# Performance work log

Measured on AMD Instinct MI355X. Metric: run time of the kernel, lower is better.

## Reference

```python
import jax, jax.numpy as jnp
import numpy as np

H = 16  # num_heads

def setup_inputs() -> dict:
    key = jax.random.key(0)
    ks = jax.random.split(key, 6)
    B, T, C, S = 2, 2048, 1024, 2048
    return {
        "q": jax.random.normal(ks[0], (B, T, C), jnp.float32),
        "k_xl": jax.random.normal(ks[1], (B, S, C), jnp.float32),
        "v_xl": jax.random.normal(ks[2], (B, S, C), jnp.float32),
        "W_qkv": jax.random.normal(ks[3], (3 * C, C), jnp.float32) * (1.0 / np.sqrt(C)),
        "W_proj": jax.random.normal(ks[4], (C, C), jnp.float32) * (1.0 / np.sqrt(C)),
        "pos_emb": jax.random.normal(ks[5], (S, C), jnp.float32),
        "is_causal": 0,
    }

def reference(q, k_xl, v_xl, W_qkv, W_proj, pos_emb, is_causal):
    B, T, C = q.shape
    hd = C // H
    # self_attention: W_qkv(q).split(d_model, -1)
    qkv = jnp.einsum('btc,dc->btd', q, W_qkv)  # [B,T,3C]
    qn, kn, vn = jnp.split(qkv, 3, axis=-1)
    # XL cache gets positional embedding added before use
    kx = k_xl + pos_emb[None, :, :]            # [B,S,C]
    vx = v_xl

    def to_heads(x):
        b, s, c = x.shape
        return x.reshape(b, s, H, hd).transpose(0, 2, 1, 3)  # [B,H,s,hd]

    qh = to_heads(qn)
    kcat = jnp.concatenate([to_heads(kx), to_heads(kn)], axis=2)  # [B,H,S+T,hd]
    vcat = jnp.concatenate([to_heads(vx), to_heads(vn)], axis=2)
    scale = 1.0 / jnp.sqrt(jnp.asarray(hd, qh.dtype))
    scores = jnp.einsum('bhtd,bhsd->bhts', qh, kcat) * scale  # [B,H,T,S+T]
    attn = jax.nn.softmax(scores, axis=-1)
    y = jnp.einsum('bhts,bhsd->bhtd', attn, vcat)  # [B,H,T,hd]
    y = y.transpose(0, 2, 1, 3).reshape(B, T, C)
    return jnp.einsum('btc,dc->btd', y, W_proj)
```

## Files before the change

### kernel.cpp

```cpp
#include <hip/hip_runtime.h>

typedef unsigned short u16;
typedef unsigned int u32;
typedef u16 u16x4 __attribute__((ext_vector_type(4)));
typedef u16 u16x8 __attribute__((ext_vector_type(8)));
typedef __bf16 bf16x8 __attribute__((ext_vector_type(8)));
typedef float f32x4 __attribute__((ext_vector_type(4)));
typedef float f32x16 __attribute__((ext_vector_type(16)));

static __device__ __forceinline__ u16 f2bf(float f) {
  union { float f; u32 u; } x; x.f = f;
  u32 r = x.u + 0x7fffu + ((x.u >> 16) & 1u);
  return (u16)(r >> 16);
}
static __device__ __forceinline__ u32 packbf(float a, float b) {
  union { u32 u; __bf16 h[2]; } x; x.h[0] = (__bf16)a; x.h[1] = (__bf16)b; return x.u;
}
static __device__ __forceinline__ void pl32swap(u32& a, u32& b) {
  asm volatile("v_permlane32_swap_b32 %0, %1" : "+v"(a), "+v"(b));
}
static __device__ __forceinline__ void gload16(const void* g, void* l) {
  __builtin_amdgcn_global_load_lds((const __attribute__((address_space(1))) unsigned int*)g,
                                   (__attribute__((address_space(3))) unsigned int*)l, 16, 0, 0);
}

__global__ __launch_bounds__(256) void cvt_fuse(const float* __restrict__ q, const float* __restrict__ wqkv_f,
                                                const float* __restrict__ wproj_f, const float* __restrict__ k_xl,
                                                const float* __restrict__ pos, u16* __restrict__ qbf,
                                                u16* __restrict__ wqkv, u16* __restrict__ wproj,
                                                u16* __restrict__ khxl, float sc) {
  int i = blockIdx.x * 256 + threadIdx.x;
  if (i < 2097152) {
    const float* src;
    u16* dst;
    int j;
    float s = 1.0f;
    if (i < 1048576) { src = q; dst = qbf; j = i; }
    else if (i < 1835008) { j = i - 1048576; src = wqkv_f; dst = wqkv; if (j < 262144) s = sc; }
    else { j = i - 1835008; src = wproj_f; dst = wproj; }
    float4 v = reinterpret_cast<const float4*>(src)[j];
    u16x4 o; o[0] = f2bf(v.x * s); o[1] = f2bf(v.y * s); o[2] = f2bf(v.z * s); o[3] = f2bf(v.w * s);
    reinterpret_cast<u16x4*>(dst)[j] = o;
  } else {
    int idx = i - 2097152;
    int d8 = idx & 7;
    int s = (idx >> 3) & 2047;
    int bh = idx >> 14;
    int b = bh >> 4, h = bh & 15;
    size_t src = ((size_t)(b * 2048 + s)) * 1024 + h * 64 + d8 * 8;
    size_t ps = ((size_t)s) * 1024 + h * 64 + d8 * 8;
    float4 a0 = *(const float4*)&k_xl[src];
    float4 a1 = *(const float4*)&k_xl[src + 4];
    float4 p0 = *(const float4*)&pos[ps];
    float4 p1 = *(const float4*)&pos[ps + 4];
    u16x8 o;
    o[0] = f2bf(a0.x + p0.x); o[1] = f2bf(a0.y + p0.y); o[2] = f2bf(a0.z + p0.z); o[3] = f2bf(a0.w + p0.w);
    o[4] = f2bf(a1.x + p1.x); o[5] = f2bf(a1.y + p1.y); o[6] = f2bf(a1.z + p1.z); o[7] = f2bf(a1.w + p1.w);
    *(u16x8*)&khxl[((size_t)bh * 2048 + s) * 64 + d8 * 8] = o;
  }
}

template <int OUT_BF16>
__global__ __launch_bounds__(256, 2) void gemm_bt3(const u16* __restrict__ A, const u16* __restrict__ B,
                                                   void* __restrict__ Cout, int M, int N, int K) {
  __shared__ alignas(128) u16 As[2][8192];
  __shared__ alignas(128) u16 Bs[2][8192];
  const int tid = threadIdx.x;
  const int m0 = blockIdx.y * 128, n0 = blockIdx.x * 128;
  const int wid = tid >> 6, lane = tid & 63;
  const int lm = lane & 15, lg = lane >> 4;
  const int wm = (wid >> 1) * 64, wn = (wid & 1) * 64;
  int srow[4], scol[4], dsto[4];
#pragma unroll
  for (int i = 0; i < 4; i++) {
    int li = tid + i * 256;
    srow[i] = li >> 3;
    scol[i] = ((li & 7) ^ (srow[i] & 7)) * 8;
    dsto[i] = (i * 256 + wid * 64) * 8;
  }
  f32x4 acc[4][4] = {};
#pragma unroll
  for (int i = 0; i < 4; i++) {
    gload16(&A[(size_t)(m0 + srow[i]) * K + scol[i]], &As[0][dsto[i]]);
    gload16(&B[(size_t)(n0 + srow[i]) * K + scol[i]], &Bs[0][dsto[i]]);
  }
  int cur = 0;
  for (int k0 = 0; k0 < K; k0 += 64) {
    __syncthreads();
    if (k0 + 64 < K) {
#pragma unroll
      for (int i = 0; i < 4; i++) {
        gload16(&A[(size_t)(m0 + srow[i]) * K + k0 + 64 + scol[i]], &As[cur ^ 1][dsto[i]]);
        gload16(&B[(size_t)(n0 + srow[i]) * K + k0 + 64 + scol[i]], &Bs[cur ^ 1][dsto[i]]);
      }
    }
    const u16* Asb = As[cur];
    const u16* Bsb = Bs[cur];
#pragma unroll
    for (int ks = 0; ks < 2; ks++) {
      bf16x8 af[4], bfr[4];
#pragma unroll
      for (int mi = 0; mi < 4; mi++) {
        int row = wm + mi * 16 + lm;
        af[mi] = *(const bf16x8*)&Asb[row * 64 + (((ks * 4 + lg) ^ (row & 7)) << 3)];
      }
#pragma unroll
      for (int ni = 0; ni < 4; ni++) {
        int row = wn + ni * 16 + lm;
        bfr[ni] = *(const bf16x8*)&Bsb[row * 64 + (((ks * 4 + lg) ^ (row & 7)) << 3)];
      }
#pragma unroll
      for (int mi = 0; mi < 4; mi++)
#pragma unroll
        for (int ni = 0; ni < 4; ni++)
          acc[mi][ni] = __builtin_amdgcn_mfma_f32_16x16x32_bf16(af[mi], bfr[ni], acc[mi][ni], 0, 0, 0);
    }
    cur ^= 1;
  }
#pragma unroll
  for (int mi = 0; mi < 4; mi++)
#pragma unroll
    for (int ni = 0; ni < 4; ni++)
#pragma unroll
      for (int r = 0; r < 4; r++) {
        int row = m0 + wm + mi * 16 + lg * 4 + r;
        int col = n0 + wn + ni * 16 + lm;
        if (OUT_BF16) ((u16*)Cout)[(size_t)row * N + col] = f2bf(acc[mi][ni][r]);
        else          ((float*)Cout)[(size_t)row * N + col] = acc[mi][ni][r];
      }
}

__global__ __launch_bounds__(256) void build_vt(const float* __restrict__ v_xl, const u16* __restrict__ qkvb,
                                                u16* __restrict__ Vt) {
  __shared__ u16 tile[64][72];
  const int bh = blockIdx.y, b = bh >> 4, h = bh & 15;
  const int s0 = blockIdx.x * 64;
  const int tid = threadIdx.x;
  {
    int sl = tid >> 2;
    int dseg = (tid & 3) * 16;
    if (s0 < 2048) {
      const float* src = v_xl + ((size_t)(b * 2048 + s0 + sl)) * 1024 + h * 64 + dseg;
#pragma unroll
      for (int j = 0; j < 16; j += 4) {
        float4 v = *(const float4*)&src[j];
        tile[sl][dseg + j] = f2bf(v.x);
        tile[sl][dseg + j + 1] = f2bf(v.y);
        tile[sl][dseg + j + 2] = f2bf(v.z);
        tile[sl][dseg + j + 3] = f2bf(v.w);
      }
    } else {
      const u16* src = qkvb + ((size_t)(b * 2048 + s0 - 2048 + sl)) * 3072 + 2048 + h * 64 + dseg;
      *(u16x8*)&tile[sl][dseg] = *(const u16x8*)&src[0];
      *(u16x8*)&tile[sl][dseg + 8] = *(const u16x8*)&src[8];
    }
  }
  __syncthreads();
  {
    int d = tid >> 2;
    int sseg = (tid & 3) * 16;
    u16* dst = Vt + ((size_t)bh * 64 + d) * 4096 + s0 + sseg;
    u16x8 o0, o1;
#pragma unroll
    for (int j = 0; j < 8; j++) { o0[j] = tile[sseg + j][d]; o1[j] = tile[sseg + 8 + j][d]; }
    *(u16x8*)&dst[0] = o0;
    *(u16x8*)&dst[8] = o1;
  }
}

__global__ __launch_bounds__(512, 4) void attn_fwd7(const u16* __restrict__ qkvb, const u16* __restrict__ khxl,
                                                    const u16* __restrict__ vt, u16* __restrict__ Y) {
  const int T = 2048;
  __shared__ alignas(128) u16 lds[16384];
  __shared__ float CBl[128];
  const int dd = blockIdx.x + (blockIdx.y << 4);
  const int w = ((dd & 7) << 6) + (dd >> 3);
  const int bh = w >> 4;
  const int q0 = (w & 15) * 128;
  const int tid = threadIdx.x, wid = tid >> 6, lane = tid & 63;
  const int qt = wid >> 1, ks = wid & 1;
  const int l31 = lane & 31, hi = lane >> 5;
  const int sw = l31 & 7;
  const int b = bh >> 4, h = bh & 15;
  const int q = q0 + qt * 32 + l31;
  const u16* Qp = qkvb + (size_t)(b * T + q) * 3072 + h * 64;
  bf16x8 qf[4];
#pragma unroll
  for (int c = 0; c < 4; c++) qf[c] = *(const bf16x8*)&Qp[c * 16 + hi * 8];
  const int srow = tid >> 3, scol = ((tid & 7) ^ (srow & 7)) * 8;
  const u16* kxl_p = khxl + ((size_t)bh * 2048 + srow) * 64 + scol;
  const u16* knew_p = qkvb + (size_t)(b * T + srow) * 3072 + 1024 + h * 64 + scol;
  const u16* v_p = vt + ((size_t)bh * 64 + srow) * 4096 + scol;
  const int dsto = tid * 8;
  f32x16 accA = {0.0f}, accB = {0.0f};
  float lrun = 0.0f;
  gload16(kxl_p, &lds[dsto]);
  gload16(v_p, &lds[8192 + dsto]);
  int cur = 0;
  const int krow = ks * 32 + l31;
  for (int t = 0; t < 64; ++t) {
    __syncthreads();
    if (t + 1 < 64) {
      const int nt = t + 1;
      const u16* ksrc = (nt < 32) ? kxl_p + (size_t)nt * 4096
                                  : knew_p + (size_t)(nt - 32) * 196608;
      gload16(ksrc, &lds[(cur ^ 1) * 4096 + dsto]);
      gload16(v_p + nt * 64, &lds[8192 + (cur ^ 1) * 4096 + dsto]);
    }
    const u16* Ksb = &lds[cur * 4096];
    const u16* Vsb = &lds[8192 + cur * 4096];
    f32x16 s = {0.0f};
    __builtin_amdgcn_s_setprio(1);
#pragma unroll
    for (int c = 0; c < 4; c++) {
      int cg = 2 * c + hi;
      bf16x8 kf = *(const bf16x8*)&Ksb[krow * 64 + ((cg ^ sw) << 3)];
      s = __builtin_amdgcn_mfma_f32_32x32x16_bf16(kf, qf[c], s, 0, 0, 0);
    }
    __builtin_amdgcn_s_setprio(0);
#pragma unroll
    for (int r = 0; r < 16; r++) s[r] = __builtin_amdgcn_exp2f(s[r]);
    float r0 = ((s[0] + s[1]) + (s[2] + s[3])) + ((s[4] + s[5]) + (s[6] + s[7]));
    float r1 = ((s[8] + s[9]) + (s[10] + s[11])) + ((s[12] + s[13]) + (s[14] + s[15]));
    lrun += r0 + r1;
    u32 w4[4][2];
#pragma unroll
    for (int g = 0; g < 4; g++) {
      w4[g][0] = packbf(s[4 * g + 0], s[4 * g + 1]);
      w4[g][1] = packbf(s[4 * g + 2], s[4 * g + 3]);
    }
    __builtin_amdgcn_s_setprio(1);
#pragma unroll
    for (int m2 = 0; m2 < 2; m2++) {
      int m = ks * 2 + m2;
      u32 W0 = w4[2 * m2][0], W2 = w4[2 * m2 + 1][0];
      pl32swap(W0, W2);
      u32 W1 = w4[2 * m2][1], W3 = w4[2 * m2 + 1][1];
      pl32swap(W1, W3);
      union { u32 u[4]; bf16x8 v; } pf;
      pf.u[0] = W0; pf.u[1] = W1; pf.u[2] = W2; pf.u[3] = W3;
      int cg = 2 * m + hi;
      bf16x8 v0 = *(const bf16x8*)&Vsb[l31 * 64 + ((cg ^ sw) << 3)];
      bf16x8 v1 = *(const bf16x8*)&Vsb[(32 + l31) * 64 + ((cg ^ sw) << 3)];
      accA = __builtin_amdgcn_mfma_f32_32x32x16_bf16(v0, pf.v, accA, 0, 0, 0);
      accB = __builtin_amdgcn_mfma_f32_32x32x16_bf16(v1, pf.v, accB, 0, 0, 0);
    }
    __builtin_amdgcn_s_setprio(0);
    cur ^= 1;
  }
  float lt = lrun + __shfl_xor(lrun, 32);
  __syncthreads();
  float* CB = (float*)lds;
  if (ks) {
    float* p = CB + (size_t)(qt * 64 + lane) * 32;
#pragma unroll
    for (int j = 0; j < 8; j++) {
      f32x4 u;
#pragma unroll
      for (int e = 0; e < 4; e++) u[e] = (j < 4) ? accA[4 * j + e] : accB[4 * (j - 4) + e];
      *(f32x4*)&p[4 * (j ^ (lane & 7))] = u;
    }
    if (hi == 0) CBl[qt * 32 + l31] = lt;
  }
  __syncthreads();
  if (!ks) {
    const float* p = CB + (size_t)(qt * 64 + lane) * 32;
#pragma unroll
    for (int j = 0; j < 8; j++) {
      f32x4 u = *(const f32x4*)&p[4 * (j ^ (lane & 7))];
#pragma unroll
      for (int e = 0; e < 4; e++) {
        if (j < 4) accA[4 * j + e] += u[e];
        else       accB[4 * (j - 4) + e] += u[e];
      }
    }
    lt += CBl[qt * 32 + l31];
    float inv = 1.0f / lt;
    u16* Ts = (u16*)((char*)lds + qt * 8192);
#pragma unroll
    for (int dt = 0; dt < 2; dt++)
#pragma unroll
      for (int r2 = 0; r2 < 4; r2++) {
        u16x4 o;
#pragma unroll
        for (int e = 0; e < 4; e++) {
          float v = dt ? accB[4 * r2 + e] : accA[4 * r2 + e];
          o[e] = f2bf(v * inv);
        }
        int dbase = dt * 32 + r2 * 8 + hi * 4;
        int byteoff = l31 * 128 + ((dbase * 2) ^ (sw << 4));
        *(u16x4*)((char*)Ts + byteoff) = o;
      }
#pragma unroll
    for (int p4 = 0; p4 < 4; p4++) {
      int row = p4 * 8 + (lane >> 3);
      int c16 = lane & 7;
      u16x8 v = *(const u16x8*)((const char*)Ts + row * 128 + ((c16 << 4) ^ ((row & 7) << 4)));
      *(u16x8*)&Y[((size_t)(b * T + q0 + qt * 32 + row)) * 1024 + h * 64 + c16 * 8] = v;
    }
  }
}

extern "C" void kernel_launch(void* const* d_in, const int* in_sizes, int n_in,
                              void* d_out, int out_size, void* d_ws, size_t ws_size,
                              hipStream_t stream) {
  const float* q = (const float*)d_in[0];
  const float* k_xl = (const float*)d_in[1];
  const float* v_xl = (const float*)d_in[2];
  const float* W_qkv = (const float*)d_in[3];
  const float* W_proj = (const float*)d_in[4];
  const float* pos = (const float*)d_in[5];

  u16* wqkv = (u16*)d_ws;
  u16* wproj = wqkv + (size_t)3072 * 1024;
  u16* qbf = wproj + (size_t)1024 * 1024;
  u16* qkvb = qbf + (size_t)4096 * 1024;
  u16* khxl = qkvb + (size_t)4096 * 3072;
  u16* vt = khxl + (size_t)4 * 1024 * 1024;
  u16* ybf = vt + (size_t)8 * 1024 * 1024;

  const float SC = 0.125f * 1.4426950408889634f;

  cvt_fuse<<<10240, 256, 0, stream>>>(q, W_qkv, W_proj, k_xl, pos, qbf, wqkv, wproj, khxl, SC);

  gemm_bt3<1><<<dim3(24, 32), 256, 0, stream>>>(qbf, wqkv, qkvb, 4096, 3072, 1024);

  build_vt<<<dim3(64, 32), 256, 0, stream>>>(v_xl, qkvb, vt);

  attn_fwd7<<<dim3(16, 32), 512, 0, stream>>>(qkvb, khxl, vt, ybf);

  gemm_bt3<0><<<dim3(8, 32), 256, 0, stream>>>(ybf, wproj, d_out, 4096, 1024, 1024);
}
```

Measured before the change: 173.6 us.

## Halve attention block to 4 waves, each computing two 32-row query tiles

The attention kernel now runs 256 threads (4 waves) per block instead of 8. Each wave holds two 32-query tiles and reuses every K and V fragment loaded from LDS for both tiles. The KV loop is manually unrolled into XL and new-token phases with double-buffered LDS staging, so the per-iteration source select goes away. This cuts LDS reads and barrier count per unit of work, at the cost of more registers per wave (four accumulators) and lower occupancy (launch bound 3).

```diff
diff --git a/kernel.cpp b/kernel.cpp
--- a/kernel.cpp
+++ b/kernel.cpp
@@ -168,7 +168,7 @@
   }
 }
 
-__global__ __launch_bounds__(512, 4) void attn_fwd7(const u16* __restrict__ qkvb, const u16* __restrict__ khxl,
+__global__ __launch_bounds__(256, 3) void attn_fwd9(const u16* __restrict__ qkvb, const u16* __restrict__ khxl,
                                                     const u16* __restrict__ vt, u16* __restrict__ Y) {
   const int T = 2048;
   __shared__ alignas(128) u16 lds[16384];
@@ -182,121 +182,202 @@
   const int l31 = lane & 31, hi = lane >> 5;
   const int sw = l31 & 7;
   const int b = bh >> 4, h = bh & 15;
-  const int q = q0 + qt * 32 + l31;
-  const u16* Qp = qkvb + (size_t)(b * T + q) * 3072 + h * 64;
-  bf16x8 qf[4];
-#pragma unroll
-  for (int c = 0; c < 4; c++) qf[c] = *(const bf16x8*)&Qp[c * 16 + hi * 8];
-  const int srow = tid >> 3, scol = ((tid & 7) ^ (srow & 7)) * 8;
-  const u16* kxl_p = khxl + ((size_t)bh * 2048 + srow) * 64 + scol;
-  const u16* knew_p = qkvb + (size_t)(b * T + srow) * 3072 + 1024 + h * 64 + scol;
-  const u16* v_p = vt + ((size_t)bh * 64 + srow) * 4096 + scol;
-  const int dsto = tid * 8;
-  f32x16 accA = {0.0f}, accB = {0.0f};
-  float lrun = 0.0f;
-  gload16(kxl_p, &lds[dsto]);
-  gload16(v_p, &lds[8192 + dsto]);
-  int cur = 0;
+  bf16x8 qf0[4], qf1[4];
+  {
+    const u16* Qp0 = qkvb + (size_t)(b * T + q0 + qt * 64 + l31) * 3072 + h * 64;
+    const u16* Qp1 = Qp0 + (size_t)32 * 3072;
+#pragma unroll
+    for (int c = 0; c < 4; c++) {
+      qf0[c] = *(const bf16x8*)&Qp0[c * 16 + hi * 8];
+      qf1[c] = *(const bf16x8*)&Qp1[c * 16 + hi * 8];
+    }
+  }
+  const int srow = tid >> 3, pc = tid & 7;
+  const int scol = (pc ^ (srow & 7)) * 8;
+  const u16* kxl_s = khxl + ((size_t)bh * 2048 + srow) * 64 + scol;
+  const u16* knew_s = qkvb + (size_t)(b * T + srow) * 3072 + 1024 + h * 64 + scol;
+  const u16* v_s = vt + ((size_t)bh * 64 + srow) * 4096 + scol;
+  const int kd = tid * 8;
+  f32x16 acc00 = {0.0f}, acc01 = {0.0f}, acc10 = {0.0f}, acc11 = {0.0f};
+  float lrun0 = 0.0f, lrun1 = 0.0f;
   const int krow = ks * 32 + l31;
-  for (int t = 0; t < 64; ++t) {
+
+#define STAGE_XL(KO, VO)                              \
+  do {                                                \
+    gload16(kxl_s, &lds[(KO) + kd]);                  \
+    gload16(kxl_s + 2048, &lds[(KO) + 2048 + kd]);    \
+    gload16(v_s, &lds[(VO) + kd]);                    \
+    gload16(v_s + 131072, &lds[(VO) + 2048 + kd]);    \
+    kxl_s += 4096; v_s += 64;                         \
+  } while (0)
+#define STAGE_NEW(KO, VO)                             \
+  do {                                                \
+    gload16(knew_s, &lds[(KO) + kd]);                 \
+    gload16(knew_s + 98304, &lds[(KO) + 2048 + kd]);  \
+    gload16(v_s, &lds[(VO) + kd]);                    \
+    gload16(v_s + 131072, &lds[(VO) + 2048 + kd]);    \
+    knew_s += 196608; v_s += 64;                      \
+  } while (0)
+#define COMPUTE(KO, VO)                                                             \
+  do {                                                                              \
+    bf16x8 kf0 = *(const bf16x8*)&lds[(KO) + krow * 64 + (((0 + hi) ^ sw) << 3)];   \
+    bf16x8 kf1 = *(const bf16x8*)&lds[(KO) + krow * 64 + (((2 + hi) ^ sw) << 3)];   \
+    bf16x8 kf2 = *(const bf16x8*)&lds[(KO) + krow * 64 + (((4 + hi) ^ sw) << 3)];   \
+    bf16x8 kf3 = *(const bf16x8*)&lds[(KO) + krow * 64 + (((6 + hi) ^ sw) << 3)];   \
+    f32x16 s0 = {0.0f}, s1 = {0.0f};                                                \
+    __builtin_amdgcn_s_setprio(1);                                                  \
+    s0 = __builtin_amdgcn_mfma_f32_32x32x16_bf16(kf0, qf0[0], s0, 0, 0, 0);         \
+    s1 = __builtin_amdgcn_mfma_f32_32x32x16_bf16(kf0, qf1[0], s1, 0, 0, 0);         \
+    s0 = __builtin_amdgcn_mfma_f32_32x32x16_bf16(kf1, qf0[1], s0, 0, 0, 0);         \
+    s1 = __builtin_amdgcn_mfma_f32_32x32x16_bf16(kf1, qf1[1], s1, 0, 0, 0);         \
+    s0 = __builtin_amdgcn_mfma_f32_32x32x16_bf16(kf2, qf0[2], s0, 0, 0, 0);         \
+    s1 = __builtin_amdgcn_mfma_f32_32x32x16_bf16(kf2, qf1[2], s1, 0, 0, 0);         \
+    s0 = __builtin_amdgcn_mfma_f32_32x32x16_bf16(kf3, qf0[3], s0, 0, 0, 0);         \
+    s1 = __builtin_amdgcn_mfma_f32_32x32x16_bf16(kf3, qf1[3], s1, 0, 0, 0);         \
+    __builtin_amdgcn_s_setprio(0);                                                  \
+    _Pragma("unroll")                                                               \
+    for (int r = 0; r < 16; r++) {                                                  \
+      s0[r] = __builtin_amdgcn_exp2f(s0[r]);                                        \
+      s1[r] = __builtin_amdgcn_exp2f(s1[r]);                                        \
+    }                                                                               \
+    lrun0 += (((s0[0] + s0[1]) + (s0[2] + s0[3])) + ((s0[4] + s0[5]) + (s0[6] + s0[7])))         \
+           + (((s0[8] + s0[9]) + (s0[10] + s0[11])) + ((s0[12] + s0[13]) + (s0[14] + s0[15])));  \
+    lrun1 += (((s1[0] + s1[1]) + (s1[2] + s1[3])) + ((s1[4] + s1[5]) + (s1[6] + s1[7])))         \
+           + (((s1[8] + s1[9]) + (s1[10] + s1[11])) + ((s1[12] + s1[13]) + (s1[14] + s1[15])));  \
+    u32 w40[4][2], w41[4][2];                                                       \
+    _Pragma("unroll")                                                               \
+    for (int g = 0; g < 4; g++) {                                                   \
+      w40[g][0] = packbf(s0[4 * g + 0], s0[4 * g + 1]);                             \
+      w40[g][1] = packbf(s0[4 * g + 2], s0[4 * g + 3]);                             \
+      w41[g][0] = packbf(s1[4 * g + 0], s1[4 * g + 1]);                             \
+      w41[g][1] = packbf(s1[4 * g + 2], s1[4 * g + 3]);                             \
+    }                                                                               \
+    __builtin_amdgcn_s_setprio(1);                                                  \
+    _Pragma("unroll")                                                               \
+    for (int m2 = 0; m2 < 2; m2++) {                                                \
+      int cg = 2 * (ks * 2 + m2) + hi;                                              \
+      bf16x8 v0 = *(const bf16x8*)&lds[(VO) + l31 * 64 + ((cg ^ sw) << 3)];         \
+      bf16x8 v1 = *(const bf16x8*)&lds[(VO) + (32 + l31) * 64 + ((cg ^ sw) << 3)];  \
+      u32 A0 = w40[2 * m2][0], A2 = w40[2 * m2 + 1][0];                             \
+      pl32swap(A0, A2);                                                             \
+      u32 A1 = w40[2 * m2][1], A3 = w40[2 * m2 + 1][1];                             \
+      pl32swap(A1, A3);                                                             \
+      union { u32 u[4]; bf16x8 v; } pf0;                                            \
+      pf0.u[0] = A0; pf0.u[1] = A1; pf0.u[2] = A2; pf0.u[3] = A3;                   \
+      acc00 = __builtin_amdgcn_mfma_f32_32x32x16_bf16(v0, pf0.v, acc00, 0, 0, 0);   \
+      acc01 = __builtin_amdgcn_mfma_f32_32x32x16_bf16(v1, pf0.v, acc01, 0, 0, 0);   \
+      u32 B0 = w41[2 * m2][0], B2 = w41[2 * m2 + 1][0];                             \
+      pl32swap(B0, B2);                                                             \
+      u32 B1 = w41[2 * m2][1], B3 = w41[2 * m2 + 1][1];                             \
+      pl32swap(B1, B3);                                                             \
+      union { u32 u[4]; bf16x8 v; } pf1;                                            \
+      pf1.u[0] = B0; pf1.u[1] = B1; pf1.u[2] = B2; pf1.u[3] = B3;                   \
+      acc10 = __builtin_amdgcn_mfma_f32_32x32x16_bf16(v0, pf1.v, acc10, 0, 0, 0);   \
+      acc11 = __builtin_amdgcn_mfma_f32_32x32x16_bf16(v1, pf1.v, acc11, 0, 0, 0);   \
+    }                                                                               \
+    __builtin_amdgcn_s_setprio(0);                                                  \
+  } while (0)
+
+  STAGE_XL(0, 8192);
+  for (int j = 0; j < 15; ++j) {
     __syncthreads();
-    if (t + 1 < 64) {
-      const int nt = t + 1;
-      const u16* ksrc = (nt < 32) ? kxl_p + (size_t)nt * 4096
-                                  : knew_p + (size_t)(nt - 32) * 196608;
-      gload16(ksrc, &lds[(cur ^ 1) * 4096 + dsto]);
-      gload16(v_p + nt * 64, &lds[8192 + (cur ^ 1) * 4096 + dsto]);
-    }
-    const u16* Ksb = &lds[cur * 4096];
-    const u16* Vsb = &lds[8192 + cur * 4096];
-    f32x16 s = {0.0f};
-    __builtin_amdgcn_s_setprio(1);
-#pragma unroll
-    for (int c = 0; c < 4; c++) {
-      int cg = 2 * c + hi;
-      bf16x8 kf = *(const bf16x8*)&Ksb[krow * 64 + ((cg ^ sw) << 3)];
-      s = __builtin_amdgcn_mfma_f32_32x32x16_bf16(kf, qf[c], s, 0, 0, 0);
-    }
-    __builtin_amdgcn_s_setprio(0);
-#pragma unroll
-    for (int r = 0; r < 16; r++) s[r] = __builtin_amdgcn_exp2f(s[r]);
-    float r0 = ((s[0] + s[1]) + (s[2] + s[3])) + ((s[4] + s[5]) + (s[6] + s[7]));
-    float r1 = ((s[8] + s[9]) + (s[10] + s[11])) + ((s[12] + s[13]) + (s[14] + s[15]));
-    lrun += r0 + r1;
-    u32 w4[4][2];
-#pragma unroll
-    for (int g = 0; g < 4; g++) {
-      w4[g][0] = packbf(s[4 * g + 0], s[4 * g + 1]);
-      w4[g][1] = packbf(s[4 * g + 2], s[4 * g + 3]);
-    }
-    __builtin_amdgcn_s_setprio(1);
-#pragma unroll
-    for (int m2 = 0; m2 < 2; m2++) {
-      int m = ks * 2 + m2;
-      u32 W0 = w4[2 * m2][0], W2 = w4[2 * m2 + 1][0];
-      pl32swap(W0, W2);
-      u32 W1 = w4[2 * m2][1], W3 = w4[2 * m2 + 1][1];
-      pl32swap(W1, W3);
-      union { u32 u[4]; bf16x8 v; } pf;
-      pf.u[0] = W0; pf.u[1] = W1; pf.u[2] = W2; pf.u[3] = W3;
-      int cg = 2 * m + hi;
-      bf16x8 v0 = *(const bf16x8*)&Vsb[l31 * 64 + ((cg ^ sw) << 3)];
-      bf16x8 v1 = *(const bf16x8*)&Vsb[(32 + l31) * 64 + ((cg ^ sw) << 3)];
-      accA = __builtin_amdgcn_mfma_f32_32x32x16_bf16(v0, pf.v, accA, 0, 0, 0);
-      accB = __builtin_amdgcn_mfma_f32_32x32x16_bf16(v1, pf.v, accB, 0, 0, 0);
-    }
-    __builtin_amdgcn_s_setprio(0);
-    cur ^= 1;
-  }
-  float lt = lrun + __shfl_xor(lrun, 32);
+    STAGE_XL(4096, 12288);
+    COMPUTE(0, 8192);
+    __syncthreads();
+    STAGE_XL(0, 8192);
+    COMPUTE(4096, 12288);
+  }
+  __syncthreads();
+  STAGE_XL(4096, 12288);
+  COMPUTE(0, 8192);
+  __syncthreads();
+  STAGE_NEW(0, 8192);
+  COMPUTE(4096, 12288);
+  for (int j = 0; j < 15; ++j) {
+    __syncthreads();
+    STAGE_NEW(4096, 12288);
+    COMPUTE(0, 8192);
+    __syncthreads();
+    STAGE_NEW(0, 8192);
+    COMPUTE(4096, 12288);
+  }
+  __syncthreads();
+  STAGE_NEW(4096, 12288);
+  COMPUTE(0, 8192);
+  __syncthreads();
+  COMPUTE(4096, 12288);
+#undef STAGE_XL
+#undef STAGE_NEW
+#undef COMPUTE
+
+  float lt0 = lrun0 + __shfl_xor(lrun0, 32);
+  float lt1 = lrun1 + __shfl_xor(lrun1, 32);
   __syncthreads();
   float* CB = (float*)lds;
   if (ks) {
-    float* p = CB + (size_t)(qt * 64 + lane) * 32;
+    float* p0 = CB + (size_t)(qt * 2 + 0) * 64 * 32 + (size_t)lane * 32;
+    float* p1 = CB + (size_t)(qt * 2 + 1) * 64 * 32 + (size_t)lane * 32;
 #pragma unroll
     for (int j = 0; j < 8; j++) {
-      f32x4 u;
-#pragma unroll
-      for (int e = 0; e < 4; e++) u[e] = (j < 4) ? accA[4 * j + e] : accB[4 * (j - 4) + e];
-      *(f32x4*)&p[4 * (j ^ (lane & 7))] = u;
-    }
-    if (hi == 0) CBl[qt * 32 + l31] = lt;
+      f32x4 u0, u1;
+#pragma unroll
+      for (int e = 0; e < 4; e++) {
+        u0[e] = (j < 4) ? acc00[4 * j + e] : acc01[4 * (j - 4) + e];
+        u1[e] = (j < 4) ? acc10[4 * j + e] : acc11[4 * (j - 4) + e];
+      }
+      *(f32x4*)&p0[4 * (j ^ (lane & 7))] = u0;
+      *(f32x4*)&p1[4 * (j ^ (lane & 7))] = u1;
+    }
+    if (hi == 0) {
+      CBl[(qt * 2 + 0) * 32 + l31] = lt0;
+      CBl[(qt * 2 + 1) * 32 + l31] = lt1;
+    }
   }
   __syncthreads();
   if (!ks) {
-    const float* p = CB + (size_t)(qt * 64 + lane) * 32;
+    const float* p0 = CB + (size_t)(qt * 2 + 0) * 64 * 32 + (size_t)lane * 32;
+    const float* p1 = CB + (size_t)(qt * 2 + 1) * 64 * 32 + (size_t)lane * 32;
 #pragma unroll
     for (int j = 0; j < 8; j++) {
-      f32x4 u = *(const f32x4*)&p[4 * (j ^ (lane & 7))];
+      f32x4 u0 = *(const f32x4*)&p0[4 * (j ^ (lane & 7))];
+      f32x4 u1 = *(const f32x4*)&p1[4 * (j ^ (lane & 7))];
 #pragma unroll
       for (int e = 0; e < 4; e++) {
-        if (j < 4) accA[4 * j + e] += u[e];
-        else       accB[4 * (j - 4) + e] += u[e];
-      }
-    }
-    lt += CBl[qt * 32 + l31];
-    float inv = 1.0f / lt;
-    u16* Ts = (u16*)((char*)lds + qt * 8192);
-#pragma unroll
-    for (int dt = 0; dt < 2; dt++)
-#pragma unroll
-      for (int r2 = 0; r2 < 4; r2++) {
-        u16x4 o;
-#pragma unroll
-        for (int e = 0; e < 4; e++) {
-          float v = dt ? accB[4 * r2 + e] : accA[4 * r2 + e];
-          o[e] = f2bf(v * inv);
+        if (j < 4) { acc00[4 * j + e] += u0[e]; acc10[4 * j + e] += u1[e]; }
+        else       { acc01[4 * (j - 4) + e] += u0[e]; acc11[4 * (j - 4) + e] += u1[e]; }
+      }
+    }
+    lt0 += CBl[(qt * 2 + 0) * 32 + l31];
+    lt1 += CBl[(qt * 2 + 1) * 32 + l31];
+    float inv0 = 1.0f / lt0;
+    float inv1 = 1.0f / lt1;
+#pragma unroll
+    for (int qb = 0; qb < 2; qb++) {
+      float inv = qb ? inv1 : inv0;
+      u16* Ts = (u16*)((char*)lds + (qt * 2 + qb) * 8192);
+#pragma unroll
+      for (int dt = 0; dt < 2; dt++)
+#pragma unroll
+        for (int r2 = 0; r2 < 4; r2++) {
+          u16x4 o;
+#pragma unroll
+          for (int e = 0; e < 4; e++) {
+            float v;
+            if (qb == 0) v = dt ? acc01[4 * r2 + e] : acc00[4 * r2 + e];
+            else         v = dt ? acc11[4 * r2 + e] : acc10[4 * r2 + e];
+            o[e] = f2bf(v * inv);
+          }
+          int dbase = dt * 32 + r2 * 8 + hi * 4;
+          int byteoff = l31 * 128 + ((dbase * 2) ^ (sw << 4));
+          *(u16x4*)((char*)Ts + byteoff) = o;
         }
-        int dbase = dt * 32 + r2 * 8 + hi * 4;
-        int byteoff = l31 * 128 + ((dbase * 2) ^ (sw << 4));
-        *(u16x4*)((char*)Ts + byteoff) = o;
-      }
-#pragma unroll
-    for (int p4 = 0; p4 < 4; p4++) {
-      int row = p4 * 8 + (lane >> 3);
-      int c16 = lane & 7;
-      u16x8 v = *(const u16x8*)((const char*)Ts + row * 128 + ((c16 << 4) ^ ((row & 7) << 4)));
-      *(u16x8*)&Y[((size_t)(b * T + q0 + qt * 32 + row)) * 1024 + h * 64 + c16 * 8] = v;
+#pragma unroll
+      for (int p4 = 0; p4 < 4; p4++) {
+        int row = p4 * 8 + (lane >> 3);
+        int c16 = lane & 7;
+        u16x8 v = *(const u16x8*)((const char*)Ts + row * 128 + ((c16 << 4) ^ ((row & 7) << 4)));
+        *(u16x8*)&Y[((size_t)(b * T + q0 + qt * 64 + qb * 32 + row)) * 1024 + h * 64 + c16 * 8] = v;
+      }
     }
   }
 }
@@ -327,7 +408,7 @@
 
   build_vt<<<dim3(64, 32), 256, 0, stream>>>(v_xl, qkvb, vt);
 
-  attn_fwd7<<<dim3(16, 32), 512, 0, stream>>>(qkvb, khxl, vt, ybf);
+  attn_fwd9<<<dim3(16, 32), 256, 0, stream>>>(qkvb, khxl, vt, ybf);
 
   gemm_bt3<0><<<dim3(8, 32), 256, 0, stream>>>(ybf, wproj, d_out, 4096, 1024, 1024);
 }
```

Result: slower. 229.6 us (+32.2%).
